# Kernel tuning notes

Hardware: AMD Instinct MI355X
Metric: run time of the kernel (lower is better)

## Reference

```python
import jax, jax.numpy as jnp
import numpy as np

H = 1024      # hidden_dim
NH = 16       # num_heads
HD = H // NH  # head_dim
EPS = 1e-12
SCALE = float(np.sqrt(H))


def setup_inputs() -> dict:
    key = jax.random.key(0)
    ks = jax.random.split(key, 12)
    S, B = 2048, 2
    inp = {
        "query": jax.random.normal(ks[0], (S, B, 2 * H), jnp.float32),
        "key":   jax.random.normal(ks[1], (S, B, H), jnp.float32),
        "value": jax.random.normal(ks[2], (S, B, H), jnp.float32),
        # gating params (zeros in torch init, but randomize for a meaningful test)
        "qs": jax.random.normal(ks[3], (1, 1, H), jnp.float32) * 0.02,
        "ks_p": jax.random.normal(ks[4], (1, 1, H), jnp.float32) * 0.02,
        "vs": jax.random.normal(ks[5], (1, 1, H), jnp.float32) * 0.02,
        # Overparam vq: Linear(H, 2H)
        "vq_w": jax.random.normal(ks[6], (2 * H, H), jnp.float32) * (1.0 / np.sqrt(H)),
        "vq_b": jax.random.normal(ks[7], (2 * H,), jnp.float32) * 0.02,
        # q_linear: Linear(2H, H)
        "ql_w": jax.random.normal(ks[8], (H, 2 * H), jnp.float32) * (1.0 / np.sqrt(2 * H)),
        "ql_b": jax.random.normal(ks[9], (H,), jnp.float32) * 0.02,
        # LayerNorm(H)
        "ln_g": jnp.ones((H,), jnp.float32),
        "ln_b": jnp.zeros((H,), jnp.float32),
    }
    return inp


def _layernorm(x, g, b):
    mu = jnp.mean(x, axis=-1, keepdims=True)
    var = jnp.mean(jnp.square(x - mu), axis=-1, keepdims=True)
    return (x - mu) * jax.lax.rsqrt(var + EPS) * g + b


def reference(query, key, value, qs, ks_p, vs, vq_w, vq_b, ql_w, ql_b, ln_g, ln_b):
    # gate vectors
    qsig = jax.nn.sigmoid(qs)            # [1,1,H]
    ksig = jax.nn.sigmoid(ks_p)          # [1,1,H]
    # vq = Overparam(sigmoid(vs)): c,f = l1(x).split(H); sigmoid(f)*tanh(c)
    h = jax.nn.sigmoid(vs) @ vq_w.T + vq_b   # [1,1,2H]
    c, f = h[..., :H], h[..., H:]
    vsig = jax.nn.sigmoid(f) * jnp.tanh(c)   # [1,1,H]

    q = qsig * _layernorm(query @ ql_w.T + ql_b, ln_g, ln_b)  # [S,B,H]
    k = ksig * key
    v = vsig * value

    # batch-first
    q = jnp.transpose(q, (1, 0, 2))  # [B,Q,H]
    k = jnp.transpose(k, (1, 0, 2))  # [B,K,H]
    v = jnp.transpose(v, (1, 0, 2))
    B, Q, _ = q.shape
    K = k.shape[1]

    qh = q.reshape(B, Q, NH, HD)
    kh = k.reshape(B, K, NH, HD)
    vh = v.reshape(B, K, NH, HD)

    scores = jnp.einsum('bqhd,bkhd->bhqk', qh, kh) / SCALE
    w = jax.nn.softmax(scores, axis=-1)                # [B,NH,Q,K]
    out = jnp.einsum('bhqk,bkhd->bqhd', w, vh).reshape(B, Q, H)
    # torch code's final .transpose(0,1) is not assigned -> output is [Q,B,H]
    return jnp.transpose(out, (1, 0, 2))
```

## Files before the change

### kernel.cpp

```cpp
#include <hip/hip_runtime.h>

typedef __bf16 bf16x8 __attribute__((ext_vector_type(8)));
typedef float f32x4 __attribute__((ext_vector_type(4)));
typedef unsigned short u16x8 __attribute__((ext_vector_type(8)));
typedef unsigned short u16x4 __attribute__((ext_vector_type(4)));
typedef unsigned short u16;
typedef unsigned int u32;


#define LOG2E 1.4426950408889634f

__device__ __forceinline__ float b2f(u16 u) {
  union { unsigned int i; float f; } x; x.i = ((unsigned int)u) << 16; return x.f;
}
__device__ __forceinline__ u16 f2b(float f) {
  union { float f; unsigned int i; } x; x.f = f;
  unsigned int r = (x.i + 0x7fffu + ((x.i >> 16) & 1u)) >> 16;
  return (u16)r;
}
__device__ __forceinline__ float sigm(float x) { return 1.0f / (1.0f + __expf(-x)); }
__device__ __forceinline__ u32 cvtpk(float lo, float hi) {
  u32 r; asm("v_cvt_pk_bf16_f32 %0, %1, %2" : "=v"(r) : "v"(lo), "v"(hi)); return r;
}

__device__ __forceinline__ void async16(u16* lds, const u16* g) {
  __builtin_amdgcn_global_load_lds((const __attribute__((address_space(1))) void*)g,
                                   (__attribute__((address_space(3))) void*)lds, 16, 0, 0);
}

__global__ __launch_bounds__(256) void k_cvt_all(const float4* __restrict__ q, u16x4* __restrict__ qd,
                                                 const float4* __restrict__ w, u16x4* __restrict__ wd,
                                                 const float4* __restrict__ k, u16x4* __restrict__ kd,
                                                 const float4* __restrict__ v, u16x4* __restrict__ vd) {
  int b = blockIdx.x;
  const float4* s; u16x4* d; int i;
  if (b < 8192)       { s = q; d = qd; i = b * 256 + threadIdx.x; }
  else if (b < 10240) { s = w; d = wd; i = (b - 8192) * 256 + threadIdx.x; }
  else if (b < 14336) { s = k; d = kd; i = (b - 10240) * 256 + threadIdx.x; }
  else                { s = v; d = vd; i = (b - 14336) * 256 + threadIdx.x; }
  float4 x = s[i];
  u16x4 o; o[0] = f2b(x.x); o[1] = f2b(x.y); o[2] = f2b(x.z); o[3] = f2b(x.w);
  d[i] = o;
}

__global__ __launch_bounds__(256) void k_h(const float* __restrict__ vs,
                                           const float* __restrict__ vq_w,
                                           const float* __restrict__ vq_b,
                                           float* __restrict__ h) {
  __shared__ float svs[1024];
  int t = threadIdx.x;
  for (int i = t; i < 1024; i += 256) svs[i] = sigm(vs[i]);
  __syncthreads();
  int wave = t >> 6, lane = t & 63;
  int row = blockIdx.x * 4 + wave;
  const float4* w4 = (const float4*)(vq_w + (size_t)row * 1024);
  const float4* s4 = (const float4*)svs;
  float acc = 0.f;
#pragma unroll
  for (int k = 0; k < 4; ++k) {
    float4 w = w4[k * 64 + lane];
    float4 s = s4[k * 64 + lane];
    acc += w.x * s.x + w.y * s.y + w.z * s.z + w.w * s.w;
  }
#pragma unroll
  for (int off = 1; off < 64; off <<= 1) acc += __shfl_xor(acc, off);
  if (lane == 0) h[row] = acc + vq_b[row];
}

__global__ __launch_bounds__(256) void k_gemm(const u16* __restrict__ A,
                                              const u16* __restrict__ Bt,
                                              u16* __restrict__ C) {
  __shared__ __align__(16) u16 As[128 * 32];
  __shared__ __align__(16) u16 Bs[128 * 32];
  int tid = threadIdx.x;
  int wave = tid >> 6, lane = tid & 63;
  int l15 = lane & 15, quad = lane >> 4;
  int bx = blockIdx.x & 255;
  int kh = blockIdx.x >> 8;
  int kofs = kh << 10;
  int m0 = (bx >> 3) * 128;
  int n0 = (bx & 7) * 128;
  int wm = (wave >> 1) * 64, wn = (wave & 1) * 64;
  f32x4 acc[4][4] = {};
  int c1 = tid, c2 = tid + 256;
  const u16* ga1 = A + (size_t)(m0 + (c1 >> 2)) * 2048 + kofs + (c1 & 3) * 8;
  const u16* ga2 = A + (size_t)(m0 + (c2 >> 2)) * 2048 + kofs + (c2 & 3) * 8;
  const u16* gb1 = Bt + (size_t)(n0 + (c1 >> 2)) * 2048 + kofs + (c1 & 3) * 8;
  const u16* gb2 = Bt + (size_t)(n0 + (c2 >> 2)) * 2048 + kofs + (c2 & 3) * 8;
  u16* lA1 = As + wave * 512;
  u16* lA2 = As + 2048 + wave * 512;
  u16* lB1 = Bs + wave * 512;
  u16* lB2 = Bs + 2048 + wave * 512;
  for (int kt = 0; kt < 32; ++kt) {
    async16(lA1, ga1); async16(lA2, ga2);
    async16(lB1, gb1); async16(lB2, gb2);
    ga1 += 32; ga2 += 32; gb1 += 32; gb2 += 32;
    __syncthreads();
    bf16x8 af[4], bfr[4];
#pragma unroll
    for (int mt = 0; mt < 4; ++mt)
      af[mt] = *(const bf16x8*)(As + (wm + mt * 16 + l15) * 32 + quad * 8);
#pragma unroll
    for (int nt = 0; nt < 4; ++nt)
      bfr[nt] = *(const bf16x8*)(Bs + (wn + nt * 16 + l15) * 32 + quad * 8);
#pragma unroll
    for (int mt = 0; mt < 4; ++mt)
#pragma unroll
      for (int nt = 0; nt < 4; ++nt)
        acc[mt][nt] = __builtin_amdgcn_mfma_f32_16x16x32_bf16(af[mt], bfr[nt], acc[mt][nt], 0, 0, 0);
    __syncthreads();
  }
  u16* Cp = C + (size_t)kh * 4096 * 1024;
#pragma unroll
  for (int mt = 0; mt < 4; ++mt) {
#pragma unroll
    for (int r = 0; r < 4; ++r) {
      int m = m0 + wm + mt * 16 + quad * 4 + r;
      u16* crow = Cp + (size_t)m * 1024 + n0 + wn + l15;
#pragma unroll
      for (int nt = 0; nt < 4; ++nt) crow[nt * 16] = f2b(acc[mt][nt][r]);
    }
  }
}

__global__ __launch_bounds__(256) void k_ln(const u16* __restrict__ qpre0,
                                            const u16* __restrict__ qpre1,
                                            const float* __restrict__ ql_b,
                                            const float* __restrict__ ln_g,
                                            const float* __restrict__ ln_b,
                                            const float* __restrict__ qs,
                                            const float* __restrict__ ks,
                                            u16* __restrict__ qatt) {
  int row = blockIdx.x;
  int t = threadIdx.x;
  u16x4 a4 = *(const u16x4*)(qpre0 + (size_t)row * 1024 + t * 4);
  u16x4 b4 = *(const u16x4*)(qpre1 + (size_t)row * 1024 + t * 4);
  float v[4];
  float s = 0.f, ss = 0.f;
#pragma unroll
  for (int j = 0; j < 4; ++j) {
    v[j] = b2f(a4[j]) + b2f(b4[j]) + ql_b[t * 4 + j];
    s += v[j]; ss += v[j] * v[j];
  }
#pragma unroll
  for (int off = 1; off < 64; off <<= 1) { s += __shfl_xor(s, off); ss += __shfl_xor(ss, off); }
  __shared__ float red[8];
  int wv = t >> 6, ln = t & 63;
  if (ln == 0) { red[wv] = s; red[4 + wv] = ss; }
  __syncthreads();
  s = red[0] + red[1] + red[2] + red[3];
  ss = red[4] + red[5] + red[6] + red[7];
  float mu = s * (1.f / 1024.f);
  float rstd = rsqrtf(ss * (1.f / 1024.f) - mu * mu + 1e-12f);
  int sidx = row >> 1, b = row & 1;
  int ch0 = t * 4;
  int hh = ch0 >> 6, hd0 = ch0 & 63;
  u16* dst = qatt + ((size_t)(b * 16 + hh) * 2048 + sidx) * 64 + hd0;
#pragma unroll
  for (int j = 0; j < 4; ++j) {
    int ch = ch0 + j;
    float gate = sigm(qs[ch]) * sigm(ks[ch]) * (LOG2E / 32.0f);
    float y = (v[j] - mu) * rstd * ln_g[ch] + ln_b[ch];
    dst[j] = f2b(y * gate);
  }
}

__device__ __forceinline__ f32x4 mfma16(bf16x8 a, bf16x8 b, f32x4 c) {
  return __builtin_amdgcn_mfma_f32_16x16x32_bf16(a, b, c, 0, 0, 0);
}

template <int CUR>
__device__ __forceinline__ void attn_iter(bool pref,
                                          bf16x8 (&kC)[4][2], bf16x8 (&kN)[4][2],
                                          const bf16x8 (&qf)[2][2],
                                          const u16* (&kp)[4], const u16*& vp,
                                          u16 (&Vt)[2][64 * 64],
                                          f32x4 (&oacc)[2][4], float (&l_i)[2],
                                          int chbase, int pcol, int l15, int colA, int colB) {
  f32x4 sacc[2][4] = {};
#pragma unroll
  for (int nt = 0; nt < 4; ++nt) {
    bf16x8 k0 = kC[nt][0], k1 = kC[nt][1];
    sacc[0][nt] = mfma16(k0, qf[0][0], sacc[0][nt]);
    sacc[0][nt] = mfma16(k1, qf[0][1], sacc[0][nt]);
    sacc[1][nt] = mfma16(k0, qf[1][0], sacc[1][nt]);
    sacc[1][nt] = mfma16(k1, qf[1][1], sacc[1][nt]);
  }
  u16x8 va, vq;
  if (pref) {
#pragma unroll
    for (int nt = 0; nt < 4; ++nt) {
      kp[nt] += 64 * 2048;
      kN[nt][0] = *(const bf16x8*)kp[nt];
      kN[nt][1] = *(const bf16x8*)(kp[nt] + 32);
    }
    vp += 64 * 2048;
    va = *(const u16x8*)vp;
    vq = *(const u16x8*)(vp + 2048);
  }
  u32 pw[2][8];
#pragma unroll
  for (int f = 0; f < 2; ++f) {
    float pe[4][4];
    float ls = 0.f;
#pragma unroll
    for (int nt = 0; nt < 4; ++nt) {
#pragma unroll
      for (int r = 0; r < 4; ++r) pe[nt][r] = __builtin_amdgcn_exp2f(sacc[f][nt][r]);
      ls += (pe[nt][0] + pe[nt][1]) + (pe[nt][2] + pe[nt][3]);
    }
    l_i[f] += ls;
    pw[f][0] = cvtpk(pe[0][0], pe[0][1]); pw[f][1] = cvtpk(pe[0][2], pe[0][3]);
    pw[f][2] = cvtpk(pe[1][0], pe[1][1]); pw[f][3] = cvtpk(pe[1][2], pe[1][3]);
    pw[f][4] = cvtpk(pe[2][0], pe[2][1]); pw[f][5] = cvtpk(pe[2][2], pe[2][3]);
    pw[f][6] = cvtpk(pe[3][0], pe[3][1]); pw[f][7] = cvtpk(pe[3][2], pe[3][3]);
  }
  union U8 { u32 w[4]; bf16x8 v; };
  bf16x8 pa[2][2];
#pragma unroll
  for (int f = 0; f < 2; ++f) {
    U8 t0; t0.w[0] = pw[f][0]; t0.w[1] = pw[f][1]; t0.w[2] = pw[f][2]; t0.w[3] = pw[f][3];
    U8 t1; t1.w[0] = pw[f][4]; t1.w[1] = pw[f][5]; t1.w[2] = pw[f][6]; t1.w[3] = pw[f][7];
    pa[f][0] = t0.v; pa[f][1] = t1.v;
  }
  const u16* vt0 = Vt[CUR];
#pragma unroll
  for (int nt = 0; nt < 4; ++nt) {
    const u16* vrow = vt0 + (nt * 16 + l15) * 64;
    bf16x8 vA = *(const bf16x8*)(vrow + colA);
    bf16x8 vB = *(const bf16x8*)(vrow + colB);
    oacc[0][nt] = mfma16(pa[0][0], vA, oacc[0][nt]);
    oacc[0][nt] = mfma16(pa[0][1], vB, oacc[0][nt]);
    oacc[1][nt] = mfma16(pa[1][0], vA, oacc[1][nt]);
    oacc[1][nt] = mfma16(pa[1][1], vB, oacc[1][nt]);
  }
  if (pref) {
    u16* vd = (u16*)Vt[CUR ^ 1];
#pragma unroll
    for (int c = 0; c < 8; ++c) {
      u32 pk2 = (u32)va[c] | ((u32)vq[c] << 16);
      *(u32*)&vd[(chbase + c) * 64 + (pcol ^ (c << 3))] = pk2;
    }
  }
  __syncthreads();
}

__global__ __launch_bounds__(256, 2) void k_attn(const u16* __restrict__ qatt,
                                                 const u16* __restrict__ key,
                                                 const u16* __restrict__ value,
                                                 const float* __restrict__ hbuf,
                                                 float* __restrict__ out) {
  int bh = blockIdx.x & 31;
  int qt = blockIdx.x >> 5;
  int b = bh >> 4, h = bh & 15;
  int tid = threadIdx.x, wave = tid >> 6, lane = tid & 63;
  int l15 = lane & 15, quad = lane >> 4;
  int q0 = qt * 128;

  __shared__ __align__(16) u16 Vt[2][64 * 64];

  bf16x8 qf[2][2];
#pragma unroll
  for (int f = 0; f < 2; ++f) {
    const u16* qrow = qatt + ((size_t)bh * 2048 + q0 + f * 64 + wave * 16 + l15) * 64 + quad * 8;
    qf[f][0] = *(const bf16x8*)qrow;
    qf[f][1] = *(const bf16x8*)(qrow + 32);
  }

  const u16* kb = key + (size_t)b * 1024 + (size_t)h * 64;
  const u16* vb = value + (size_t)b * 1024 + (size_t)h * 64;

  const u16* kp[4];
#pragma unroll
  for (int nt = 0; nt < 4; ++nt) kp[nt] = kb + (size_t)(nt * 16 + l15) * 2048 + quad * 8;

  int p = lane & 31;
  int chbase = wave * 16 + (lane >> 5) * 8;
  const u16* vp = vb + (size_t)2 * p * 2048 + chbase;
  int kk = 2 * p;
  int pcol = ((kk >> 5) & 1) * 32 + ((kk >> 2) & 3) * 8 + ((kk >> 4) & 1) * 4 + (kk & 3);
  int swr = (l15 & 7) << 3;
  int colA = (8 * quad) ^ swr;
  int colB = (32 + 8 * quad) ^ swr;

  bf16x8 kA[4][2], kB[4][2];
#pragma unroll
  for (int nt = 0; nt < 4; ++nt) {
    kA[nt][0] = *(const bf16x8*)kp[nt];
    kA[nt][1] = *(const bf16x8*)(kp[nt] + 32);
  }
  {
    u16x8 va = *(const u16x8*)vp;
    u16x8 vq = *(const u16x8*)(vp + 2048);
#pragma unroll
    for (int c = 0; c < 8; ++c) {
      u32 pk2 = (u32)va[c] | ((u32)vq[c] << 16);
      *(u32*)&Vt[0][(chbase + c) * 64 + (pcol ^ (c << 3))] = pk2;
    }
  }
  __syncthreads();

  f32x4 oacc[2][4] = {};
  float l_i[2] = {};

  for (int kt = 0; kt < 32; kt += 2) {
    attn_iter<0>(true, kA, kB, qf, kp, vp, Vt, oacc, l_i, chbase, pcol, l15, colA, colB);
    attn_iter<1>(kt < 30, kB, kA, qf, kp, vp, Vt, oacc, l_i, chbase, pcol, l15, colA, colB);
  }

#pragma unroll
  for (int f = 0; f < 2; ++f) {
    float l = l_i[f];
    l += __shfl_xor(l, 16);
    l += __shfl_xor(l, 32);
    l_i[f] = l;
  }
  float vsg[4];
#pragma unroll
  for (int nt = 0; nt < 4; ++nt) {
    int ch = h * 64 + nt * 16 + l15;
    vsg[nt] = sigm(hbuf[1024 + ch]) * tanhf(hbuf[ch]);
  }
#pragma unroll
  for (int f = 0; f < 2; ++f)
#pragma unroll
    for (int r = 0; r < 4; ++r) {
      int sq = q0 + f * 64 + wave * 16 + quad * 4 + r;
      float inv = 1.0f / __shfl(l_i[f], quad * 4 + r);
      float* orow = out + ((size_t)sq * 2 + b) * 1024 + h * 64;
#pragma unroll
      for (int nt = 0; nt < 4; ++nt)
        orow[nt * 16 + l15] = oacc[f][nt][r] * inv * vsg[nt];
    }
}

extern "C" void kernel_launch(void* const* d_in, const int* in_sizes, int n_in,
                              void* d_out, int out_size, void* d_ws, size_t ws_size,
                              hipStream_t stream) {
  (void)in_sizes; (void)n_in; (void)out_size; (void)ws_size;
  const float* query = (const float*)d_in[0];
  const float* key   = (const float*)d_in[1];
  const float* value = (const float*)d_in[2];
  const float* qs    = (const float*)d_in[3];
  const float* ksp   = (const float*)d_in[4];
  const float* vs    = (const float*)d_in[5];
  const float* vq_w  = (const float*)d_in[6];
  const float* vq_b  = (const float*)d_in[7];
  const float* ql_w  = (const float*)d_in[8];
  const float* ql_b  = (const float*)d_in[9];
  const float* ln_g  = (const float*)d_in[10];
  const float* ln_b  = (const float*)d_in[11];
  float* out = (float*)d_out;

  float* ws = (float*)d_ws;
  float* h   = ws;
  u16* qpre  = (u16*)(ws + 4096);
  u16* qbf   = qpre + (size_t)2 * 4096 * 1024;
  u16* qatt  = qbf;
  u16* wbf   = qbf + (size_t)4096 * 2048;
  u16* kbf   = wbf + (size_t)1024 * 2048;
  u16* vbf   = kbf + (size_t)4096 * 1024;

  hipLaunchKernelGGL(k_cvt_all, dim3(18432), dim3(256), 0, stream,
                     (const float4*)query, (u16x4*)qbf,
                     (const float4*)ql_w,  (u16x4*)wbf,
                     (const float4*)key,   (u16x4*)kbf,
                     (const float4*)value, (u16x4*)vbf);
  hipLaunchKernelGGL(k_h,    dim3(512),  dim3(256), 0, stream, vs, vq_w, vq_b, h);
  hipLaunchKernelGGL(k_gemm, dim3(512),  dim3(256), 0, stream, qbf, wbf, qpre);
  hipLaunchKernelGGL(k_ln,   dim3(4096), dim3(256), 0, stream, qpre, qpre + (size_t)4096 * 1024,
                     ql_b, ln_g, ln_b, qs, ksp, qatt);
  hipLaunchKernelGGL(k_attn, dim3(512),  dim3(256), 0, stream, qatt, kbf, vbf, h, out);
}
```

Measured before the change: 258.4 us.

## Stage K tiles through swizzled shared memory instead of per-wave register loads

Each block now loads its K tile once into a double-buffered, XOR-swizzled LDS buffer shared by all waves. Previously each wave fetched the full K tile from global memory into registers. This cuts redundant global K traffic and frees the K prefetch registers. In exchange it adds LDS writes and reads per iteration and doubles shared memory use, which may limit occupancy.

```diff
diff --git a/kernel.cpp b/kernel.cpp
--- a/kernel.cpp
+++ b/kernel.cpp
@@ -171,29 +171,29 @@
 
 template <int CUR>
 __device__ __forceinline__ void attn_iter(bool pref,
-                                          bf16x8 (&kC)[4][2], bf16x8 (&kN)[4][2],
                                           const bf16x8 (&qf)[2][2],
-                                          const u16* (&kp)[4], const u16*& vp,
-                                          u16 (&Vt)[2][64 * 64],
+                                          const u16*& kp, const u16*& vp,
+                                          u16 (&Ks)[2][64 * 64], u16 (&Vt)[2][64 * 64],
                                           f32x4 (&oacc)[2][4], float (&l_i)[2],
-                                          int chbase, int pcol, int l15, int colA, int colB) {
+                                          int kdst, int chbase, int pcol,
+                                          int l15, int colA, int colB) {
   f32x4 sacc[2][4] = {};
+  const u16* kt0 = Ks[CUR];
 #pragma unroll
   for (int nt = 0; nt < 4; ++nt) {
-    bf16x8 k0 = kC[nt][0], k1 = kC[nt][1];
-    sacc[0][nt] = mfma16(k0, qf[0][0], sacc[0][nt]);
-    sacc[0][nt] = mfma16(k1, qf[0][1], sacc[0][nt]);
-    sacc[1][nt] = mfma16(k0, qf[1][0], sacc[1][nt]);
-    sacc[1][nt] = mfma16(k1, qf[1][1], sacc[1][nt]);
-  }
-  u16x8 va, vq;
+    const u16* krow = kt0 + (nt * 16 + l15) * 64;
+    bf16x8 kA = *(const bf16x8*)(krow + colA);
+    bf16x8 kB = *(const bf16x8*)(krow + colB);
+    sacc[0][nt] = mfma16(kA, qf[0][0], sacc[0][nt]);
+    sacc[0][nt] = mfma16(kB, qf[0][1], sacc[0][nt]);
+    sacc[1][nt] = mfma16(kA, qf[1][0], sacc[1][nt]);
+    sacc[1][nt] = mfma16(kB, qf[1][1], sacc[1][nt]);
+  }
+  u16x8 kr0, kr1, va, vq;
   if (pref) {
-#pragma unroll
-    for (int nt = 0; nt < 4; ++nt) {
-      kp[nt] += 64 * 2048;
-      kN[nt][0] = *(const bf16x8*)kp[nt];
-      kN[nt][1] = *(const bf16x8*)(kp[nt] + 32);
-    }
+    kp += 64 * 2048;
+    kr0 = *(const u16x8*)kp;
+    kr1 = *(const u16x8*)(kp + (size_t)32 * 2048);
     vp += 64 * 2048;
     va = *(const u16x8*)vp;
     vq = *(const u16x8*)(vp + 2048);
@@ -235,6 +235,9 @@
     oacc[1][nt] = mfma16(pa[1][1], vB, oacc[1][nt]);
   }
   if (pref) {
+    u16* kd = (u16*)Ks[CUR ^ 1];
+    *(u16x8*)(kd + kdst) = kr0;
+    *(u16x8*)(kd + kdst + 2048) = kr1;
     u16* vd = (u16*)Vt[CUR ^ 1];
 #pragma unroll
     for (int c = 0; c < 8; ++c) {
@@ -257,6 +260,7 @@
   int l15 = lane & 15, quad = lane >> 4;
   int q0 = qt * 128;
 
+  __shared__ __align__(16) u16 Ks[2][64 * 64];
   __shared__ __align__(16) u16 Vt[2][64 * 64];
 
   bf16x8 qf[2][2];
@@ -270,9 +274,10 @@
   const u16* kb = key + (size_t)b * 1024 + (size_t)h * 64;
   const u16* vb = value + (size_t)b * 1024 + (size_t)h * 64;
 
-  const u16* kp[4];
-#pragma unroll
-  for (int nt = 0; nt < 4; ++nt) kp[nt] = kb + (size_t)(nt * 16 + l15) * 2048 + quad * 8;
+  int krow = tid >> 3;
+  int kchk = (tid & 7) * 8;
+  const u16* kp = kb + (size_t)krow * 2048 + kchk;
+  int kdst = krow * 64 + (kchk ^ ((krow & 7) << 3));
 
   int p = lane & 31;
   int chbase = wave * 16 + (lane >> 5) * 8;
@@ -283,13 +288,11 @@
   int colA = (8 * quad) ^ swr;
   int colB = (32 + 8 * quad) ^ swr;
 
-  bf16x8 kA[4][2], kB[4][2];
-#pragma unroll
-  for (int nt = 0; nt < 4; ++nt) {
-    kA[nt][0] = *(const bf16x8*)kp[nt];
-    kA[nt][1] = *(const bf16x8*)(kp[nt] + 32);
-  }
   {
+    u16x8 kr0 = *(const u16x8*)kp;
+    u16x8 kr1 = *(const u16x8*)(kp + (size_t)32 * 2048);
+    *(u16x8*)(&Ks[0][kdst]) = kr0;
+    *(u16x8*)(&Ks[0][kdst + 2048]) = kr1;
     u16x8 va = *(const u16x8*)vp;
     u16x8 vq = *(const u16x8*)(vp + 2048);
 #pragma unroll
@@ -304,8 +307,8 @@
   float l_i[2] = {};
 
   for (int kt = 0; kt < 32; kt += 2) {
-    attn_iter<0>(true, kA, kB, qf, kp, vp, Vt, oacc, l_i, chbase, pcol, l15, colA, colB);
-    attn_iter<1>(kt < 30, kB, kA, qf, kp, vp, Vt, oacc, l_i, chbase, pcol, l15, colA, colB);
+    attn_iter<0>(true, qf, kp, vp, Ks, Vt, oacc, l_i, kdst, chbase, pcol, l15, colA, colB);
+    attn_iter<1>(kt < 30, qf, kp, vp, Ks, Vt, oacc, l_i, kdst, chbase, pcol, l15, colA, colB);
   }
 
 #pragma unroll
```

Measured after the change: 222.0 us. 1.16x faster.
